# Performance work log

Measured on AMD Instinct MI355X. Metric: run time of the kernel, lower is better.

## Reference

```python
import jax, jax.numpy as jnp
import numpy as np

# --- model dims (from init args) ---
LAYERS = 6
LEAF = 2 ** (LAYERS - 1)        # 32
M_LEN = 128
CAM_NUM = 2
MAIN_CAM = 0
LATENT = 48
H_LAT = 2048                    # LatentNet hidden
H_BR = 512                      # ChooseBranchNet hidden
B = 16384

# Path bits: for leaf i, bit at classifier depth d (root->leaf order) is
# (i >> (LAYERS-2-d)) & 1. This is exactly what the search_table + double
# advanced-indexing gather in the torch code computes (heap tree routing).
_BITS = ((np.arange(LEAF)[:, None] >> np.arange(LAYERS - 2, -1, -1)[None, :]) & 1)  # [LEAF, LAYERS-1]
BITS = jnp.asarray(_BITS, dtype=jnp.int32)


def setup_inputs() -> dict:
    key = jax.random.key(0)
    ks = jax.random.split(key, 9)
    s = lambda fan: 1.0 / np.sqrt(fan)
    return {
        "batch_data": jax.random.normal(ks[0], (B, CAM_NUM, M_LEN), dtype=jnp.float32),
        # LatentNet: [B, 2*M_LEN] -> hidden -> LEAF*LATENT
        "Wl1": jax.random.normal(ks[1], (2 * M_LEN, H_LAT), dtype=jnp.float32) * s(2 * M_LEN),
        "bl1": jnp.zeros((H_LAT,), dtype=jnp.float32),
        "Wl2": jax.random.normal(ks[2], (H_LAT, LEAF * LATENT), dtype=jnp.float32) * s(H_LAT),
        "bl2": jnp.zeros((LEAF * LATENT,), dtype=jnp.float32),
        # ChooseBranchNet (shared across the LAYERS-1 classifier slots): M_LEN -> hidden -> 2
        "Wb1": jax.random.normal(ks[3], (M_LEN, H_BR), dtype=jnp.float32) * s(M_LEN),
        "bb1": jnp.zeros((H_BR,), dtype=jnp.float32),
        "Wb2": jax.random.normal(ks[4], (H_BR, 2), dtype=jnp.float32) * s(H_BR),
        "bb2": jnp.zeros((2,), dtype=jnp.float32),
    }


def reference(batch_data, Wl1, bl1, Wl2, bl2, Wb1, bb1, Wb2, bb2):
    bsz = batch_data.shape[0]
    # expand_measurements: main cam repeated (LAYERS-1) times -> [B, LAYERS-1, M_LEN]
    main = batch_data[:, MAIN_CAM]                                  # [B, M_LEN]
    x_br = jnp.broadcast_to(main[:, None, :], (bsz, LAYERS - 1, M_LEN))
    # ChooseBranchNet -> per-layer 2-way probabilities
    h = jax.nn.relu(jnp.einsum('blm,mh->blh', x_br, Wb1) + bb1)
    p = jax.nn.softmax(jnp.einsum('blh,ho->blo', h, Wb2) + bb2, axis=-1)  # [B, L-1, 2]
    # Tree gates: product of path-branch probabilities along root->leaf path.
    comp = jnp.where(BITS[None] == 1, p[:, None, :, 1], p[:, None, :, 0])  # [B, LEAF, L-1]
    gates = jnp.prod(comp, axis=-1)                                        # [B, LEAF]
    # top-1 routing (argsort(...)[:, -1] as in the torch code)
    router = jnp.argsort(gates, axis=-1)[:, -1]                            # [B]
    # LatentNet on concatenated two-camera measurements
    x2 = jnp.concatenate([batch_data[:, 0], batch_data[:, 1]], axis=-1)    # [B, 2*M_LEN]
    hl = jax.nn.relu(x2 @ Wl1 + bl1)
    nn_latent = (hl @ Wl2 + bl2).reshape(bsz, LEAF, LATENT)
    # scatter-select per-sample leaf latent (replaces the torch.where loop)
    select = jnp.take_along_axis(nn_latent, router[:, None, None], axis=1)[:, 0]  # [B, LATENT]
    return select
```

## Files before the change

kernel.cpp:

```cpp
#include <hip/hip_runtime.h>
#include <stdint.h>

typedef short bf16x8 __attribute__((ext_vector_type(8)));
typedef float f32x4 __attribute__((ext_vector_type(4)));

#define NROWS 16384
#define K1DIM 256
#define N1DIM 2048
#define N2DIM 96
#define MARGIN 0.03f

#define GLD16(g, l) __builtin_amdgcn_global_load_lds( \
    (const __attribute__((address_space(1))) uint32_t*)(g), \
    (__attribute__((address_space(3))) uint32_t*)(l), 16, 0, 0)

__device__ __forceinline__ ushort f2bf(float x) {
  union { float f; uint32_t u; } c; c.f = x;
  uint32_t u = c.u;
  return (ushort)((u + 0x7FFFu + ((u >> 16) & 1u)) >> 16);
}

__global__ __launch_bounds__(256) void k0_convert(
    const float* __restrict__ bd, const float* __restrict__ Wl1,
    const float* __restrict__ Wl2, const float* __restrict__ Wb1,
    ushort* __restrict__ x2bf, ushort* __restrict__ wl1t,
    ushort* __restrict__ w2t, ushort* __restrict__ wb1t) {
  int i = blockIdx.x * 256 + threadIdx.x;
  if (i < NROWS * 256) x2bf[i] = f2bf(bd[i]);
  if (i < 2048 * 256) {
    int n = i >> 8, k = i & 255;
    wl1t[i] = f2bf(Wl1[k * 2048 + n]);
  }
  if (i < 96 * 2048) {
    int j = i >> 11, k = i & 2047;
    int col = (j < 48) ? j : (1440 + j);
    w2t[i] = f2bf(Wl2[k * 1536 + col]);
  }
  if (i < 512 * 128) {
    int j = i >> 7, m = i & 127;
    wb1t[i] = f2bf(Wb1[m * 512 + j]);
  }
}

__global__ __launch_bounds__(256) void k1a_score(
    const ushort* __restrict__ x2bf, const ushort* __restrict__ wb1t,
    const float* __restrict__ bb1, const float* __restrict__ Wb2,
    float* __restrict__ part) {
  __shared__ __align__(1024) ushort As[128 * 64];
  __shared__ __align__(1024) ushort Bs[128 * 64];
  const int t = threadIdx.x, ln = t & 63, wv = t >> 6;
  const int m0 = blockIdx.y << 7;
  const int n0 = blockIdx.x << 7;
  const int wm = (wv >> 1) << 6, wn = (wv & 1) << 6;
  const int rsub = ln >> 3, kc8 = ln & 7;
  const int q = ln >> 4, rr = ln & 15;

  f32x4 acc[4][4] = {};

  for (int k0 = 0; k0 < 128; k0 += 64) {
#pragma unroll
    for (int i = 0; i < 4; i++) {
      int inst = (wv << 2) + i;
      int row = (inst << 3) + rsub;
      GLD16(x2bf + (size_t)(m0 + row) * 256 + k0 + (kc8 << 3), As + (inst << 9));
      GLD16(wb1t + (size_t)(n0 + row) * 128 + k0 + (kc8 << 3), Bs + (inst << 9));
    }
    __syncthreads();
#pragma unroll
    for (int kk = 0; kk < 2; kk++) {
      int kb = ((kk << 2) + q) << 3;
      bf16x8 af[4], bfr[4];
#pragma unroll
      for (int mi = 0; mi < 4; mi++)
        af[mi] = *(const bf16x8*)(As + (((wm + (mi << 4) + rr)) << 6) + kb);
#pragma unroll
      for (int ni = 0; ni < 4; ni++)
        bfr[ni] = *(const bf16x8*)(Bs + (((wn + (ni << 4) + rr)) << 6) + kb);
#pragma unroll
      for (int mi = 0; mi < 4; mi++)
#pragma unroll
        for (int ni = 0; ni < 4; ni++)
          acc[mi][ni] = __builtin_amdgcn_mfma_f32_16x16x32_bf16(
              af[mi], bfr[ni], acc[mi][ni], 0, 0, 0);
    }
    __syncthreads();
  }

  float s4[4][4] = {};
#pragma unroll
  for (int ni = 0; ni < 4; ni++) {
    int col = n0 + wn + (ni << 4) + rr;
    float bias = bb1[col];
    float wdv = Wb2[col * 2 + 1] - Wb2[col * 2];
#pragma unroll
    for (int mi = 0; mi < 4; mi++) {
      f32x4 a = acc[mi][ni];
#pragma unroll
      for (int v = 0; v < 4; v++)
        s4[mi][v] += fmaxf(a[v] + bias, 0.f) * wdv;
    }
  }
#pragma unroll
  for (int off = 1; off <= 8; off <<= 1)
#pragma unroll
    for (int mi = 0; mi < 4; mi++)
#pragma unroll
      for (int v = 0; v < 4; v++)
        s4[mi][v] += __shfl_xor(s4[mi][v], off);

  if (rr == 0) {
    float* dst = part + (size_t)(blockIdx.x * 2 + (wv & 1)) * NROWS +
                 m0 + wm + (q << 2);
#pragma unroll
    for (int mi = 0; mi < 4; mi++) {
      float4 v4 = make_float4(s4[mi][0], s4[mi][1], s4[mi][2], s4[mi][3]);
      *(float4*)(dst + (mi << 4)) = v4;
    }
  }
}

__global__ __launch_bounds__(256) void k1b_classify(
    const float* __restrict__ part, const float* __restrict__ bb2,
    int* __restrict__ router, int* __restrict__ list, int* __restrict__ counter) {
  int t = blockIdx.x * 256 + threadIdx.x;
  float s = bb2[1] - bb2[0];
#pragma unroll
  for (int i = 0; i < 8; i++) s += part[i * NROWS + t];
  router[t] = (s >= 0.f) ? 1 : 0;
  if (fabsf(s) < MARGIN) {
    int idx = atomicAdd(counter, 1);
    list[idx] = t;
  }
}

__global__ __launch_bounds__(256) void k1c_recheck(
    const float* __restrict__ bd, const float* __restrict__ Wb1,
    const float* __restrict__ Wb2, const float* __restrict__ bb1,
    const float* __restrict__ bb2, const int* __restrict__ list,
    const int* __restrict__ counter, int* __restrict__ router) {
  const int ln = threadIdx.x & 63;
  const int wid = (blockIdx.x * 256 + threadIdx.x) >> 6;
  const int count = *counter;
  const float c = bb2[1] - bb2[0];

  for (int base = wid * 4; base < count; base += 512 * 4) {
    int rows[4];
#pragma unroll
    for (int r = 0; r < 4; r++) {
      int idx = base + r;
      rows[r] = list[(idx < count) ? idx : base];
    }
    float acc[4][8];
#pragma unroll
    for (int r = 0; r < 4; r++)
#pragma unroll
      for (int u = 0; u < 8; u++) acc[r][u] = 0.f;

    for (int m = 0; m < 128; m++) {
      float w[8];
#pragma unroll
      for (int u = 0; u < 8; u++) w[u] = Wb1[m * 512 + (u << 6) + ln];
#pragma unroll
      for (int r = 0; r < 4; r++) {
        float x = bd[(size_t)rows[r] * 256 + m];
#pragma unroll
        for (int u = 0; u < 8; u++) acc[r][u] = fmaf(x, w[u], acc[r][u]);
      }
    }
    float sc[4];
#pragma unroll
    for (int r = 0; r < 4; r++) {
      float s = 0.f;
#pragma unroll
      for (int u = 0; u < 8; u++) {
        int j = (u << 6) + ln;
        float wd = Wb2[j * 2 + 1] - Wb2[j * 2];
        s += fmaxf(acc[r][u] + bb1[j], 0.f) * wd;
      }
#pragma unroll
      for (int off = 1; off <= 32; off <<= 1) s += __shfl_xor(s, off);
      sc[r] = s + c;
    }
    if (ln == 0) {
#pragma unroll
      for (int r = 0; r < 4; r++)
        if (base + r < count) router[rows[r]] = (sc[r] >= 0.f) ? 1 : 0;
    }
  }
}

__global__ __launch_bounds__(256) void k2_fused(
    const ushort* __restrict__ x2bf, const ushort* __restrict__ wl1t,
    const ushort* __restrict__ w2t, const float* __restrict__ bl1,
    float* __restrict__ P) {
  __shared__ __align__(1024) ushort As[64 * 64];
  __shared__ __align__(1024) ushort Bs[128 * 64];
  __shared__ __align__(1024) ushort Ws[2 * 96 * 64];
  __shared__ __align__(1024) ushort Hs[64 * 136];
  const int t = threadIdx.x, ln = t & 63, wv = t >> 6;
  const int ks2 = blockIdx.x;
  const int m0 = blockIdx.y << 6;
  const int q = ln >> 4, rr = ln & 15;
  const int rsub = ln >> 3, kc8 = ln & 7;

  f32x4 accP[6] = {};

  for (int nc = 0; nc < 8; nc++) {
    const int n0 = (ks2 << 10) + (nc << 7);

#pragma unroll
    for (int j = 0; j < 6; j++) {
      int inst = wv * 6 + j;
      int h = inst / 12;
      int r0 = (inst - h * 12) << 3;
      GLD16(w2t + (size_t)(r0 + rsub) * 2048 + n0 + (h << 6) + (kc8 << 3),
            Ws + h * 6144 + ((inst - h * 12) << 9));
    }

    f32x4 acc1[4][2] = {};
    for (int k0 = 0; k0 < K1DIM; k0 += 64) {
#pragma unroll
      for (int i = 0; i < 2; i++) {
        int inst = (wv << 1) + i;
        int row = (inst << 3) + rsub;
        GLD16(x2bf + (size_t)(m0 + row) * K1DIM + k0 + (kc8 << 3),
              As + (inst << 9));
      }
#pragma unroll
      for (int i = 0; i < 4; i++) {
        int inst = (wv << 2) + i;
        int row = (inst << 3) + rsub;
        GLD16(wl1t + (size_t)(n0 + row) * K1DIM + k0 + (kc8 << 3),
              Bs + (inst << 9));
      }
      __syncthreads();
#pragma unroll
      for (int kk = 0; kk < 2; kk++) {
        int kb = (kk << 5) + (q << 3);
        bf16x8 af[4], bfr[2];
#pragma unroll
        for (int mi = 0; mi < 4; mi++)
          af[mi] = *(const bf16x8*)(As + (((mi << 4) + rr) << 6) + kb);
#pragma unroll
        for (int ni = 0; ni < 2; ni++)
          bfr[ni] = *(const bf16x8*)(Bs + (((wv << 5) + (ni << 4) + rr) << 6) + kb);
#pragma unroll
        for (int mi = 0; mi < 4; mi++)
#pragma unroll
          for (int ni = 0; ni < 2; ni++)
            acc1[mi][ni] = __builtin_amdgcn_mfma_f32_16x16x32_bf16(
                af[mi], bfr[ni], acc1[mi][ni], 0, 0, 0);
      }
      __syncthreads();
    }

#pragma unroll
    for (int ni = 0; ni < 2; ni++) {
      int lcol = (wv << 5) + (ni << 4) + rr;
      float bias = bl1[n0 + lcol];
#pragma unroll
      for (int mi = 0; mi < 4; mi++) {
        f32x4 a = acc1[mi][ni];
#pragma unroll
        for (int v = 0; v < 4; v++) {
          int lrow = (mi << 4) + (q << 2) + v;
          Hs[lrow * 136 + lcol] = f2bf(fmaxf(a[v] + bias, 0.f));
        }
      }
    }
    __syncthreads();

#pragma unroll
    for (int kk = 0; kk < 4; kk++) {
      int half = kk >> 1;
      int k64 = (kk & 1) << 5;
      bf16x8 ha = *(const bf16x8*)(Hs + ((wv << 4) + rr) * 136 + (kk << 5) + (q << 3));
#pragma unroll
      for (int ni = 0; ni < 6; ni++) {
        bf16x8 wb = *(const bf16x8*)(Ws + half * 6144 +
                                     (((ni << 4) + rr) << 6) + k64 + (q << 3));
        accP[ni] = __builtin_amdgcn_mfma_f32_16x16x32_bf16(ha, wb, accP[ni], 0, 0, 0);
      }
    }
    __syncthreads();
  }

#pragma unroll
  for (int ni = 0; ni < 6; ni++) {
#pragma unroll
    for (int v = 0; v < 4; v++) {
      int row = m0 + (wv << 4) + (q << 2) + v;
      int col = (ni << 4) + rr;
      P[(size_t)ks2 * NROWS * N2DIM + (size_t)row * N2DIM + col] = accP[ni][v];
    }
  }
}

__global__ __launch_bounds__(256) void k3_select(
    const float* __restrict__ P0, const float* __restrict__ P1,
    const float* __restrict__ bl2, const int* __restrict__ router,
    float* __restrict__ out) {
  int t = blockIdx.x * 256 + threadIdx.x;
  int b = t / 12, i4 = (t % 12) * 4;
  int sel = router[b];
  int cb = sel ? 48 : 0;
  int bb = sel ? 1488 : 0;
  float4 p0 = *(const float4*)(P0 + (size_t)b * N2DIM + cb + i4);
  float4 p1 = *(const float4*)(P1 + (size_t)b * N2DIM + cb + i4);
  float4 bz = *(const float4*)(bl2 + bb + i4);
  float4 r;
  r.x = p0.x + p1.x + bz.x;
  r.y = p0.y + p1.y + bz.y;
  r.z = p0.z + p1.z + bz.z;
  r.w = p0.w + p1.w + bz.w;
  *(float4*)(out + (size_t)b * 48 + i4) = r;
}

extern "C" void kernel_launch(void* const* d_in, const int* in_sizes, int n_in,
                              void* d_out, int out_size, void* d_ws, size_t ws_size,
                              hipStream_t stream) {
  const float* bd  = (const float*)d_in[0];
  const float* Wl1 = (const float*)d_in[1];
  const float* bl1 = (const float*)d_in[2];
  const float* Wl2 = (const float*)d_in[3];
  const float* bl2 = (const float*)d_in[4];
  const float* Wb1 = (const float*)d_in[5];
  const float* bb1 = (const float*)d_in[6];
  const float* Wb2 = (const float*)d_in[7];
  const float* bb2 = (const float*)d_in[8];

  char* ws = (char*)d_ws;
  ushort* x2bf  = (ushort*)(ws);
  ushort* wl1t  = (ushort*)(ws + 8388608);
  ushort* w2t   = (ushort*)(ws + 9437184);
  float*  P     = (float*)(ws + 76939264);
  int*    router= (int*)(ws + 89522176);
  ushort* wb1t  = (ushort*)(ws + 89587712);
  float*  part  = (float*)(ws + 89718784);
  int*    list  = (int*)(ws + 90243072);
  int*    counter=(int*)(ws + 90308608);
  float*  outp  = (float*)d_out;

  k0_convert<<<dim3(16384), dim3(256), 0, stream>>>(bd, Wl1, Wl2, Wb1,
                                                    x2bf, wl1t, w2t, wb1t);
  hipMemsetAsync(counter, 0, 4, stream);
  k1a_score<<<dim3(4, 128), dim3(256), 0, stream>>>(x2bf, wb1t, bb1, Wb2, part);
  k1b_classify<<<dim3(64), dim3(256), 0, stream>>>(part, bb2, router, list, counter);
  k1c_recheck<<<dim3(128), dim3(256), 0, stream>>>(bd, Wb1, Wb2, bb1, bb2,
                                                   list, counter, router);
  k2_fused<<<dim3(2, 256), dim3(256), 0, stream>>>(x2bf, wl1t, w2t, bl1, P);
  k3_select<<<dim3(768), dim3(256), 0, stream>>>(P, P + (size_t)NROWS * N2DIM, bl2,
                                                 router, outp);
}
```

Measured before the change: 186.5 us.

## Fuse select epilogue into GEMM kernel with atomics and XOR-swizzle LDS tiles

The separate k3_select kernel and its P workspace are removed. The fused GEMM epilogue now picks the router-selected leaf columns, adds bl2 in the first K-split, and atomically accumulates into a zeroed output. In addition, the LDS layouts for the A, B, W and H tiles use an XOR swizzle instead of padding, to avoid bank conflicts. The change trades the extra kernel launch and the P round-trip for a memset plus fp32 atomics, which also make the summation order nondeterministic.

```diff
diff --git a/kernel.cpp b/kernel.cpp
--- a/kernel.cpp
+++ b/kernel.cpp
@@ -192,16 +192,18 @@
 __global__ __launch_bounds__(256) void k2_fused(
     const ushort* __restrict__ x2bf, const ushort* __restrict__ wl1t,
     const ushort* __restrict__ w2t, const float* __restrict__ bl1,
-    float* __restrict__ P) {
+    const float* __restrict__ bl2, const int* __restrict__ router,
+    float* __restrict__ out) {
   __shared__ __align__(1024) ushort As[64 * 64];
   __shared__ __align__(1024) ushort Bs[128 * 64];
   __shared__ __align__(1024) ushort Ws[2 * 96 * 64];
-  __shared__ __align__(1024) ushort Hs[64 * 136];
+  __shared__ __align__(1024) ushort Hs[64 * 128];
   const int t = threadIdx.x, ln = t & 63, wv = t >> 6;
   const int ks2 = blockIdx.x;
   const int m0 = blockIdx.y << 6;
   const int q = ln >> 4, rr = ln & 15;
-  const int rsub = ln >> 3, kc8 = ln & 7;
+  const int rsub = ln >> 3;
+  const int swz8 = ((ln & 7) ^ rsub) << 3;
 
   f32x4 accP[6] = {};
 
@@ -212,9 +214,9 @@
     for (int j = 0; j < 6; j++) {
       int inst = wv * 6 + j;
       int h = inst / 12;
-      int r0 = (inst - h * 12) << 3;
-      GLD16(w2t + (size_t)(r0 + rsub) * 2048 + n0 + (h << 6) + (kc8 << 3),
-            Ws + h * 6144 + ((inst - h * 12) << 9));
+      int r12 = inst - h * 12;
+      GLD16(w2t + (size_t)((r12 << 3) + rsub) * 2048 + n0 + (h << 6) + swz8,
+            Ws + h * 6144 + (r12 << 9));
     }
 
     f32x4 acc1[4][2] = {};
@@ -222,28 +224,28 @@
 #pragma unroll
       for (int i = 0; i < 2; i++) {
         int inst = (wv << 1) + i;
-        int row = (inst << 3) + rsub;
-        GLD16(x2bf + (size_t)(m0 + row) * K1DIM + k0 + (kc8 << 3),
+        GLD16(x2bf + (size_t)(m0 + (inst << 3) + rsub) * K1DIM + k0 + swz8,
               As + (inst << 9));
       }
 #pragma unroll
       for (int i = 0; i < 4; i++) {
         int inst = (wv << 2) + i;
-        int row = (inst << 3) + rsub;
-        GLD16(wl1t + (size_t)(n0 + row) * K1DIM + k0 + (kc8 << 3),
+        GLD16(wl1t + (size_t)(n0 + (inst << 3) + rsub) * K1DIM + k0 + swz8,
               Bs + (inst << 9));
       }
       __syncthreads();
 #pragma unroll
       for (int kk = 0; kk < 2; kk++) {
-        int kb = (kk << 5) + (q << 3);
+        int slot = ((kk << 2) + q);
         bf16x8 af[4], bfr[2];
 #pragma unroll
         for (int mi = 0; mi < 4; mi++)
-          af[mi] = *(const bf16x8*)(As + (((mi << 4) + rr) << 6) + kb);
+          af[mi] = *(const bf16x8*)(As + (((mi << 4) + rr) << 6) +
+                                    ((slot ^ (rr & 7)) << 3));
 #pragma unroll
         for (int ni = 0; ni < 2; ni++)
-          bfr[ni] = *(const bf16x8*)(Bs + (((wv << 5) + (ni << 4) + rr) << 6) + kb);
+          bfr[ni] = *(const bf16x8*)(Bs + (((wv << 5) + (ni << 4) + rr) << 6) +
+                                     ((slot ^ (rr & 7)) << 3));
 #pragma unroll
         for (int mi = 0; mi < 4; mi++)
 #pragma unroll
@@ -257,6 +259,7 @@
 #pragma unroll
     for (int ni = 0; ni < 2; ni++) {
       int lcol = (wv << 5) + (ni << 4) + rr;
+      int slotc = lcol >> 3;
       float bias = bl1[n0 + lcol];
 #pragma unroll
       for (int mi = 0; mi < 4; mi++) {
@@ -264,7 +267,8 @@
 #pragma unroll
         for (int v = 0; v < 4; v++) {
           int lrow = (mi << 4) + (q << 2) + v;
-          Hs[lrow * 136 + lcol] = f2bf(fmaxf(a[v] + bias, 0.f));
+          Hs[(lrow << 7) + ((slotc ^ (lrow & 15)) << 3) + (rr & 7)] =
+              f2bf(fmaxf(a[v] + bias, 0.f));
         }
       }
     }
@@ -273,47 +277,42 @@
 #pragma unroll
     for (int kk = 0; kk < 4; kk++) {
       int half = kk >> 1;
-      int k64 = (kk & 1) << 5;
-      bf16x8 ha = *(const bf16x8*)(Hs + ((wv << 4) + rr) * 136 + (kk << 5) + (q << 3));
+      int c2 = ((kk & 1) << 2) + q;
+      int cH = (kk << 2) + q;
+      bf16x8 ha = *(const bf16x8*)(Hs + (((wv << 4) + rr) << 7) +
+                                   ((cH ^ rr) << 3));
 #pragma unroll
       for (int ni = 0; ni < 6; ni++) {
         bf16x8 wb = *(const bf16x8*)(Ws + half * 6144 +
-                                     (((ni << 4) + rr) << 6) + k64 + (q << 3));
+                                     (((ni << 4) + rr) << 6) +
+                                     ((c2 ^ (rr & 7)) << 3));
         accP[ni] = __builtin_amdgcn_mfma_f32_16x16x32_bf16(ha, wb, accP[ni], 0, 0, 0);
       }
     }
     __syncthreads();
   }
 
-#pragma unroll
-  for (int ni = 0; ni < 6; ni++) {
+  {
+    int rowb = m0 + (wv << 4) + (q << 2);
 #pragma unroll
     for (int v = 0; v < 4; v++) {
-      int row = m0 + (wv << 4) + (q << 2) + v;
-      int col = (ni << 4) + rr;
-      P[(size_t)ks2 * NROWS * N2DIM + (size_t)row * N2DIM + col] = accP[ni][v];
-    }
-  }
-}
-
-__global__ __launch_bounds__(256) void k3_select(
-    const float* __restrict__ P0, const float* __restrict__ P1,
-    const float* __restrict__ bl2, const int* __restrict__ router,
-    float* __restrict__ out) {
-  int t = blockIdx.x * 256 + threadIdx.x;
-  int b = t / 12, i4 = (t % 12) * 4;
-  int sel = router[b];
-  int cb = sel ? 48 : 0;
-  int bb = sel ? 1488 : 0;
-  float4 p0 = *(const float4*)(P0 + (size_t)b * N2DIM + cb + i4);
-  float4 p1 = *(const float4*)(P1 + (size_t)b * N2DIM + cb + i4);
-  float4 bz = *(const float4*)(bl2 + bb + i4);
-  float4 r;
-  r.x = p0.x + p1.x + bz.x;
-  r.y = p0.y + p1.y + bz.y;
-  r.z = p0.z + p1.z + bz.z;
-  r.w = p0.w + p1.w + bz.w;
-  *(float4*)(out + (size_t)b * 48 + i4) = r;
+      int row = rowb + v;
+      int sel = router[row];
+      float v0 = sel ? accP[3][v] : accP[0][v];
+      float v1 = sel ? accP[4][v] : accP[1][v];
+      float v2 = sel ? accP[5][v] : accP[2][v];
+      if (ks2 == 0) {
+        int bb = sel ? 1488 : 0;
+        v0 += bl2[bb + rr];
+        v1 += bl2[bb + 16 + rr];
+        v2 += bl2[bb + 32 + rr];
+      }
+      float* ob = out + (size_t)row * 48 + rr;
+      atomicAdd(ob, v0);
+      atomicAdd(ob + 16, v1);
+      atomicAdd(ob + 32, v2);
+    }
+  }
 }
 
 extern "C" void kernel_launch(void* const* d_in, const int* in_sizes, int n_in,
@@ -333,7 +332,6 @@
   ushort* x2bf  = (ushort*)(ws);
   ushort* wl1t  = (ushort*)(ws + 8388608);
   ushort* w2t   = (ushort*)(ws + 9437184);
-  float*  P     = (float*)(ws + 76939264);
   int*    router= (int*)(ws + 89522176);
   ushort* wb1t  = (ushort*)(ws + 89587712);
   float*  part  = (float*)(ws + 89718784);
@@ -344,11 +342,11 @@
   k0_convert<<<dim3(16384), dim3(256), 0, stream>>>(bd, Wl1, Wl2, Wb1,
                                                     x2bf, wl1t, w2t, wb1t);
   hipMemsetAsync(counter, 0, 4, stream);
+  hipMemsetAsync(outp, 0, (size_t)out_size * 4, stream);
   k1a_score<<<dim3(4, 128), dim3(256), 0, stream>>>(x2bf, wb1t, bb1, Wb2, part);
   k1b_classify<<<dim3(64), dim3(256), 0, stream>>>(part, bb2, router, list, counter);
   k1c_recheck<<<dim3(128), dim3(256), 0, stream>>>(bd, Wb1, Wb2, bb1, bb2,
                                                    list, counter, router);
-  k2_fused<<<dim3(2, 256), dim3(256), 0, stream>>>(x2bf, wl1t, w2t, bl1, P);
-  k3_select<<<dim3(768), dim3(256), 0, stream>>>(P, P + (size_t)NROWS * N2DIM, bl2,
-                                                 router, outp);
-}
+  k2_fused<<<dim3(2, 256), dim3(256), 0, stream>>>(x2bf, wl1t, w2t, bl1, bl2,
+                                                   router, outp);
+}
```

After: 173.7 us. -6.9%, faster.
